# Kernel tuning notes

Measured on AMD Instinct MI355X. Metric: run time of the kernel, lower is better.

The kernel has to match this reference:

```python
import jax, jax.numpy as jnp
import numpy as np

N, E, G = 50000, 800000, 1024      # nodes, edges, graphs
NF, R, H, O, B = 32, 4, 64, 16, 2  # node vocab, relations, hidden, output, conv blocks
MAX_DEG = 10                       # PyG MFConv default max_degree


def setup_inputs() -> dict:
    key = jax.random.key(0)
    ks = jax.random.split(key, 32)
    s = 0.05
    inp = {
        "x": jax.random.normal(ks[0], (N, NF), jnp.float32),
        "edge_attr": jax.random.normal(ks[1], (E, R), jnp.float32),
        "edge_index": jax.random.randint(ks[2], (2, E), 0, N),
        "batch_idx": jnp.sort(jax.random.randint(ks[3], (N,), 0, G)),
        "emb": jax.random.normal(ks[4], (NF, H), jnp.float32) * s,
        "lin1_w": jax.random.normal(ks[5], (H, H), jnp.float32) * s,
        "lin1_b": jnp.zeros((H,), jnp.float32),
        "lin2_w": jax.random.normal(ks[6], (H, O), jnp.float32) * s,
        "lin2_b": jnp.zeros((O,), jnp.float32),
    }
    for b in range(B):
        k = 7 + 4 * b
        inp[f"rgcn_w{b}"] = jax.random.normal(ks[k], (R, H, H), jnp.float32) * s
        inp[f"rgcn_root{b}"] = jax.random.normal(ks[k + 1], (H, H), jnp.float32) * s
        inp[f"rgcn_b{b}"] = jnp.zeros((H,), jnp.float32)
        inp[f"mf_wl{b}"] = jax.random.normal(ks[k + 2], (MAX_DEG + 1, H, H), jnp.float32) * s
        inp[f"mf_bl{b}"] = jnp.zeros((MAX_DEG + 1, H), jnp.float32)
        inp[f"mf_wr{b}"] = jax.random.normal(ks[k + 3], (MAX_DEG + 1, H, H), jnp.float32) * s
    return inp


def _rgcn(h, src, tgt, rel, W, Wroot, bias):
    # PyG RGCNConv: per-relation linear transform + per-(node,relation) MEAN aggregation + root + bias.
    hx = jnp.einsum('nh,rho->rno', h, W)            # [R,N,H] transformed features per relation
    m = hx[rel, src]                                # [E,H] per-edge messages
    seg = tgt * R + rel                             # segment id per (target node, relation)
    cnt = jax.ops.segment_sum(jnp.ones((E,), h.dtype), seg, num_segments=N * R)
    inv = jnp.where(cnt > 0, 1.0 / cnt, 0.0)
    agg = jax.ops.segment_sum(m * inv[seg][:, None], tgt, num_segments=N)
    return agg + h @ Wroot + bias


def _mfconv(h, src, tgt, Wl, bl, Wr):
    # PyG MFConv: sum-aggregate neighbors, then degree-indexed linear layers (lin_l has bias, lin_r none).
    deg = jnp.clip(jax.ops.segment_sum(jnp.ones((E,), jnp.int32), tgt, num_segments=N), 0, MAX_DEG)
    agg = jax.ops.segment_sum(h[src], tgt, num_segments=N)   # [N,H]
    out = jnp.zeros_like(h)
    for d in range(MAX_DEG + 1):                    # fixed small set of degree buckets
        mask = (deg == d)[:, None]
        out = out + jnp.where(mask, agg @ Wl[d] + bl[d] + h @ Wr[d], 0.0)
    return out


def reference(x, edge_index, edge_attr, batch_idx, emb,
              rgcn_w0, rgcn_root0, rgcn_b0, mf_wl0, mf_bl0, mf_wr0,
              rgcn_w1, rgcn_root1, rgcn_b1, mf_wl1, mf_bl1, mf_wr1,
              lin1_w, lin1_b, lin2_w, lin2_b):
    src, tgt = edge_index[0], edge_index[1]
    rel = jnp.argmax(edge_attr, axis=-1)
    h = emb[jnp.argmax(x, axis=-1)]                 # node embedding lookup
    blocks = [(rgcn_w0, rgcn_root0, rgcn_b0, mf_wl0, mf_bl0, mf_wr0),
              (rgcn_w1, rgcn_root1, rgcn_b1, mf_wl1, mf_bl1, mf_wr1)]
    for (W, Wro, bi, Wl, bl, Wr) in blocks:
        h = jax.nn.relu(h)
        h = _rgcn(h, src, tgt, rel, W, Wro, bi)
        h = jax.nn.relu(h)
        h = _mfconv(h, src, tgt, Wl, bl, Wr)
    g = jax.ops.segment_sum(h, batch_idx, num_segments=G)   # global add pool
    g = jax.nn.relu(g @ lin1_w + lin1_b)
    return g @ lin2_w + lin2_b
```

## Files before the change

kernel.cpp:

```cpp
#include <hip/hip_runtime.h>
#include <hip/hip_fp16.h>
#include <cstdint>
#include <cstddef>

#define Nn 50000
#define Ne 800000
#define Ng 1024
#define NFd 32
#define Rr 4
#define Hd 64
#define Od 16
#define MAXD 10
#define NSEG (Nn * Rr)
#define SCAN_BLK ((NSEG + 255) / 256)
#define ORDER_SZ (Nn + 176)
#define NB_MF (ORDER_SZ / 16)
#define NB_RG (Nn / 16)
#define NB_RELSEG (Ne / 256)
#define NB_EMBED (Nn / 4)
#define WT_PER_LAYER (Hd * 5 * Hd)
#define MFWT_PER_LAYER ((MAXD + 1) * Hd * 2 * Hd)
#define PREP_TOTAL (2 * WT_PER_LAYER + 2 * MFWT_PER_LAYER)

typedef _Float16 f16x8 __attribute__((ext_vector_type(8)));
typedef float f32x4 __attribute__((ext_vector_type(4)));

__device__ __forceinline__ float reluf(float v) { return v > 0.f ? v : 0.f; }
__device__ __forceinline__ int rfl(int v) { return __builtin_amdgcn_readfirstlane(v); }

__global__ void k_rel_emb(const float4* __restrict__ ea, const int* __restrict__ eidx,
                          int* __restrict__ seg, int* __restrict__ rank,
                          int* __restrict__ cnt,
                          const float* __restrict__ x, const float* __restrict__ emb,
                          __half* __restrict__ h16) {
    if (blockIdx.x < NB_RELSEG) {
        int e = blockIdx.x * 256 + threadIdx.x;
        float4 a = ea[e];
        int bi = 0; float bv = a.x;
        if (a.y > bv) { bv = a.y; bi = 1; }
        if (a.z > bv) { bv = a.z; bi = 2; }
        if (a.w > bv) { bv = a.w; bi = 3; }
        int s = eidx[Ne + e] * Rr + bi;
        seg[e] = s;
        rank[e] = atomicAdd(&cnt[s], 1);
    } else {
        int wave = ((blockIdx.x - NB_RELSEG) * 256 + threadIdx.x) >> 6;
        int lane = threadIdx.x & 63;
        float v = (lane < NFd) ? x[(size_t)wave * NFd + lane] : -1e30f;
        int idx = lane;
        #pragma unroll
        for (int off = 16; off >= 1; off >>= 1) {
            float ov = __shfl_down(v, off);
            int oi = __shfl_down(idx, off);
            if (ov > v || (ov == v && oi < idx)) { v = ov; idx = oi; }
        }
        idx = __shfl(idx, 0);
        float hv = reluf(emb[(size_t)idx * Hd + lane]);
        h16[(size_t)wave * Hd + lane] = __float2half(hv);
    }
}

__global__ void k_prep(const float* __restrict__ w0, const float* __restrict__ r0,
                       const float* __restrict__ w1, const float* __restrict__ r1,
                       const float* __restrict__ wl0, const float* __restrict__ wr0,
                       const float* __restrict__ wl1, const float* __restrict__ wr1,
                       __half* __restrict__ wt, __half* __restrict__ mfwt) {
    int idx = blockIdx.x * 256 + threadIdx.x;
    if (idx < 2 * WT_PER_LAYER) {
        int b = idx / WT_PER_LAYER;
        int rem = idx % WT_PER_LAYER;
        int c = rem / 320;
        int k = rem % 320;
        const float* W  = b ? w1 : w0;
        const float* Rt = b ? r1 : r0;
        float v = (k < 64) ? Rt[k * Hd + c]
                           : W[((size_t)((k - 64) >> 6)) * Hd * Hd + ((k - 64) & 63) * Hd + c];
        wt[idx] = __float2half(v);
    } else if (idx < PREP_TOTAL) {
        int j = idx - 2 * WT_PER_LAYER;
        int b = j / MFWT_PER_LAYER;
        int rem = j % MFWT_PER_LAYER;
        int d = rem / (Hd * 128);
        int r2 = rem % (Hd * 128);
        int c = r2 / 128;
        int k = r2 % 128;
        const float* Wl = b ? wl1 : wl0;
        const float* Wr = b ? wr1 : wr0;
        float v = (k < 64) ? Wl[(size_t)d * Hd * Hd + k * Hd + c]
                           : Wr[(size_t)d * Hd * Hd + (k - 64) * Hd + c];
        mfwt[j] = __float2half(v);
    }
}

__global__ void k_scan1(const int* __restrict__ cnt, int* __restrict__ off,
                        int* __restrict__ bsum, int* __restrict__ bcnt) {
    __shared__ int s[256];
    __shared__ int hist[16];
    int t = threadIdx.x;
    if (t < 16) hist[t] = 0;
    int idx = blockIdx.x * 256 + t;
    int v = (idx < NSEG) ? cnt[idx] : 0;
    s[t] = v;
    __syncthreads();
    if ((t & 3) == 0 && idx < NSEG) {
        int dsum = s[t] + s[t + 1] + s[t + 2] + s[t + 3];
        atomicAdd(&hist[min(dsum, MAXD)], 1);
    }
    #pragma unroll
    for (int o = 1; o < 256; o <<= 1) {
        int x = (t >= o) ? s[t - o] : 0;
        __syncthreads();
        s[t] += x;
        __syncthreads();
    }
    if (idx < NSEG) off[idx] = s[t] - v;
    if (t == 255) bsum[blockIdx.x] = s[255];
    if (t < 16) {
        int h = hist[t];
        if (h > 0) atomicAdd(&bcnt[t], h);
    }
}

__global__ void k_scan2(int* __restrict__ bsum, const int* __restrict__ bcnt,
                        int* __restrict__ bbase, int* __restrict__ order) {
    __shared__ int s[1024];
    int t = threadIdx.x;
    int v = (t < SCAN_BLK) ? bsum[t] : 0;
    s[t] = v;
    __syncthreads();
    #pragma unroll
    for (int o = 1; o < 1024; o <<= 1) {
        int x = (t >= o) ? s[t - o] : 0;
        __syncthreads();
        s[t] += x;
        __syncthreads();
    }
    if (t < SCAN_BLK) bsum[t] = s[t] - v;
    if (t == 0) {
        int run = 0;
        for (int d = 0; d <= MAXD; d++) {
            int c = bcnt[d];
            bbase[d] = run;
            int pad = (c + 15) & ~15;
            for (int i = c; i < pad; i++) order[run + i] = -1;
            run += pad;
        }
        for (int i = run; i < ORDER_SZ; i++) order[i] = -1;
    }
}

__global__ void k_scan3_bucket(int* __restrict__ off, const int* __restrict__ bsum,
                               const int4* __restrict__ cnt4, const int* __restrict__ bbase,
                               int* __restrict__ bfill, int* __restrict__ order) {
    __shared__ int hist[16];
    __shared__ int base[16];
    int t = threadIdx.x;
    if (t < 16) hist[t] = 0;
    __syncthreads();
    int idx = blockIdx.x * 256 + t;
    if (idx == 0) off[NSEG] = Ne;
    if (idx < NSEG) off[idx] = off[idx] + bsum[blockIdx.x];
    int d = 0, rk = 0;
    bool valid = (idx < Nn);
    if (valid) {
        int4 c = cnt4[idx];
        d = min(c.x + c.y + c.z + c.w, MAXD);
        rk = atomicAdd(&hist[d], 1);
    }
    __syncthreads();
    if (t < 16) {
        int h = hist[t];
        base[t] = (h > 0) ? atomicAdd(&bfill[t], h) : 0;
    }
    __syncthreads();
    if (valid) order[bbase[d] + base[d] + rk] = idx | (d << 20);
}

__global__ void k_scatter(const int* __restrict__ eidx, const int* __restrict__ seg,
                          const int* __restrict__ rank, const int* __restrict__ off,
                          int* __restrict__ sorted_src) {
    int e = blockIdx.x * 256 + threadIdx.x;
    if (e >= Ne) return;
    int pos = off[seg[e]] + rank[e];
    sorted_src[pos] = eidx[e];
}

#define H16(ptr, s) __half2float((ptr)[(size_t)(s) * Hd + lane])

__global__ __launch_bounds__(256) void k_rgcn_fused(
        const __half* __restrict__ hin16,
        const int* __restrict__ off, const int* __restrict__ ssrc,
        const __half* __restrict__ wt, const float* __restrict__ bias,
        float* __restrict__ hout, __half* __restrict__ hout16) {
    __shared__ __align__(16) __half alds[16 * 296];
    int tid = threadIdx.x;
    int wv = tid >> 6, lane = tid & 63;
    int nblk = rfl(blockIdx.x * 16);
    int n0 = nblk + wv * 4;
    int obv = off[4 * n0 + min(lane, 16)];
    int cntv = __shfl(obv, lane + 1) - obv;
    float ivv = (cntv > 0) ? 1.f / (float)cntv : 0.f;
    int e    = rfl(__shfl(obv, 0));
    int eEnd = rfl(__shfl(obv, 16));

    float acc = 0.f, snap = 0.f;
    int segi = 0;
    int nb = rfl(__shfl(obv, 1));

#define EMIT_SEG do {                                                \
        float d_ = acc - snap; snap = acc;                           \
        float iv_ = __shfl(ivv, segi);                               \
        alds[(wv * 4 + (segi >> 2)) * 296 + (segi & 3) * 72 + lane]  \
            = __float2half(d_ * iv_);                                \
        segi++;                                                      \
        nb = (segi < 16) ? rfl(__shfl(obv, segi + 1)) : 0x7fffffff;  \
    } while (0)

    if (e + 16 <= eEnd) {
        int4 iA = *(const int4*)(ssrc + e);
        int4 iB = *(const int4*)(ssrc + e + 4);
        int4 iC = *(const int4*)(ssrc + e + 8);
        int4 iD = *(const int4*)(ssrc + e + 12);
        while (true) {
            int en = e + 16;
            bool more = (en + 16 <= eEnd);
            int4 jA, jB, jC, jD;
            if (more) {
                jA = *(const int4*)(ssrc + en);
                jB = *(const int4*)(ssrc + en + 4);
                jC = *(const int4*)(ssrc + en + 8);
                jD = *(const int4*)(ssrc + en + 12);
            }
            float v0 = H16(hin16, iA.x);
            float v1 = H16(hin16, iA.y);
            float v2 = H16(hin16, iA.z);
            float v3 = H16(hin16, iA.w);
            float v4 = H16(hin16, iB.x);
            float v5 = H16(hin16, iB.y);
            float v6 = H16(hin16, iB.z);
            float v7 = H16(hin16, iB.w);
            float v8 = H16(hin16, iC.x);
            float v9 = H16(hin16, iC.y);
            float vA = H16(hin16, iC.z);
            float vB = H16(hin16, iC.w);
            float vC = H16(hin16, iD.x);
            float vD = H16(hin16, iD.y);
            float vE = H16(hin16, iD.z);
            float vF = H16(hin16, iD.w);
            while (e + 0  == nb) EMIT_SEG;  acc += v0;
            while (e + 1  == nb) EMIT_SEG;  acc += v1;
            while (e + 2  == nb) EMIT_SEG;  acc += v2;
            while (e + 3  == nb) EMIT_SEG;  acc += v3;
            while (e + 4  == nb) EMIT_SEG;  acc += v4;
            while (e + 5  == nb) EMIT_SEG;  acc += v5;
            while (e + 6  == nb) EMIT_SEG;  acc += v6;
            while (e + 7  == nb) EMIT_SEG;  acc += v7;
            while (e + 8  == nb) EMIT_SEG;  acc += v8;
            while (e + 9  == nb) EMIT_SEG;  acc += v9;
            while (e + 10 == nb) EMIT_SEG;  acc += vA;
            while (e + 11 == nb) EMIT_SEG;  acc += vB;
            while (e + 12 == nb) EMIT_SEG;  acc += vC;
            while (e + 13 == nb) EMIT_SEG;  acc += vD;
            while (e + 14 == nb) EMIT_SEG;  acc += vE;
            while (e + 15 == nb) EMIT_SEG;  acc += vF;
            e = en;
            if (!more) break;
            iA = jA; iB = jB; iC = jC; iD = jD;
        }
    }
    for (; e < eEnd; e++) {
        while (e == nb) EMIT_SEG;
        int s = rfl(ssrc[e]);
        acc += H16(hin16, s);
    }
    while (segi < 16) EMIT_SEG;
#undef EMIT_SEG

    __syncthreads();

    int rp = lane & 15;
    int g  = lane >> 4;
    const __half* ha = hin16 + (size_t)(nblk + rp) * Hd + 8 * g;
    const __half* ba = wt + (size_t)(wv * 16 + rp) * 320 + 8 * g;
    const __half* aa = alds + rp * 296 + 8 * g;
    f32x4 dacc = {0.f, 0.f, 0.f, 0.f};
    #pragma unroll
    for (int s = 0; s < 10; s++) {
        f16x8 bfrag = *(const f16x8*)(ba + s * 32);
        f16x8 afrag;
        if (s < 2) afrag = *(const f16x8*)(ha + s * 32);
        else       afrag = *(const f16x8*)(aa + ((s - 2) >> 1) * 72 + ((s - 2) & 1) * 32);
        dacc = __builtin_amdgcn_mfma_f32_16x16x32_f16(afrag, bfrag, dacc, 0, 0, 0);
    }
    int c = wv * 16 + rp;
    float bb = bias[c];
    #pragma unroll
    for (int j = 0; j < 4; j++) {
        int row = nblk + g * 4 + j;
        float v = reluf(dacc[j] + bb);
        hout[(size_t)row * Hd + c] = v;
        hout16[(size_t)row * Hd + c] = __float2half(v);
    }
}

__global__ __launch_bounds__(256) void k_mf_fused(
        const __half* __restrict__ hin16,
        const int* __restrict__ off, const int* __restrict__ ssrc,
        const int* __restrict__ order, const __half* __restrict__ mfwt,
        const float* __restrict__ bl,
        float* __restrict__ hout, __half* __restrict__ hout16, int relu_out) {
    __shared__ __align__(16) __half alds[16 * 72];
    int tid = threadIdx.x;
    int wv = tid >> 6, lane = tid & 63;
    int blk = rfl(blockIdx.x * 16);
    int ent0 = rfl(order[blk]);
    if (ent0 < 0) return;
    int d = ent0 >> 20;
    for (int i = 0; i < 4; i++) {
        int slot = blk + wv * 4 + i;
        int ent = rfl(order[slot]);
        float sum = 0.f;
        if (ent >= 0) {
            int n = ent & 0xFFFFF;
            int e0 = rfl(off[n * Rr]);
            int e4 = rfl(off[n * Rr + Rr]);
            float p0 = 0.f, p1 = 0.f, p2 = 0.f, p3 = 0.f;
            int e = e0;
            for (; e + 16 <= e4; e += 16) {
                const int4 sA = *(const int4*)(ssrc + e);
                const int4 sB = *(const int4*)(ssrc + e + 4);
                const int4 sC = *(const int4*)(ssrc + e + 8);
                const int4 sD = *(const int4*)(ssrc + e + 12);
                p0 += H16(hin16, sA.x) + H16(hin16, sA.y) + H16(hin16, sA.z) + H16(hin16, sA.w);
                p1 += H16(hin16, sB.x) + H16(hin16, sB.y) + H16(hin16, sB.z) + H16(hin16, sB.w);
                p2 += H16(hin16, sC.x) + H16(hin16, sC.y) + H16(hin16, sC.z) + H16(hin16, sC.w);
                p3 += H16(hin16, sD.x) + H16(hin16, sD.y) + H16(hin16, sD.z) + H16(hin16, sD.w);
            }
            for (; e + 4 <= e4; e += 4) {
                const int4 sA = *(const int4*)(ssrc + e);
                p0 += H16(hin16, sA.x) + H16(hin16, sA.y) + H16(hin16, sA.z) + H16(hin16, sA.w);
            }
            for (; e < e4; e++) {
                int s = rfl(ssrc[e]);
                p0 += H16(hin16, s);
            }
            sum = (p0 + p1) + (p2 + p3);
        }
        alds[(wv * 4 + i) * 72 + lane] = __float2half(sum);
    }
    __syncthreads();

    int rp = lane & 15;
    int g  = lane >> 4;
    int entr = order[blk + rp];
    int nr = (entr >= 0) ? (entr & 0xFFFFF) : 0;
    const __half* aa = alds + rp * 72 + 8 * g;
    const __half* ha = hin16 + (size_t)nr * Hd + 8 * g;
    const __half* ba = mfwt + ((size_t)d * Hd + wv * 16 + rp) * 128 + 8 * g;
    f32x4 dacc = {0.f, 0.f, 0.f, 0.f};
    #pragma unroll
    for (int s = 0; s < 4; s++) {
        f16x8 bfrag = *(const f16x8*)(ba + s * 32);
        f16x8 afrag = (s < 2) ? *(const f16x8*)(aa + s * 32)
                              : *(const f16x8*)(ha + (s - 2) * 32);
        dacc = __builtin_amdgcn_mfma_f32_16x16x32_f16(afrag, bfrag, dacc, 0, 0, 0);
    }
    int c = wv * 16 + rp;
    float bb = bl[d * Hd + c];
    #pragma unroll
    for (int j = 0; j < 4; j++) {
        int entw = order[blk + g * 4 + j];
        if (entw >= 0) {
            int n = entw & 0xFFFFF;
            float v = dacc[j] + bb;
            if (relu_out) {
                v = reluf(v);
                hout16[(size_t)n * Hd + c] = __float2half(v);
            }
            hout[(size_t)n * Hd + c] = v;
        }
    }
}

__global__ void k_pool(const float* __restrict__ h, const int* __restrict__ batch,
                       float* __restrict__ g) {
    int wave = rfl((blockIdx.x * 256 + threadIdx.x) >> 6);
    int lane = threadIdx.x & 63;
    int n0 = wave * 4;
    if (n0 >= Nn) return;
    int b0 = batch[n0], b1 = batch[n0 + 1], b2 = batch[n0 + 2], b3 = batch[n0 + 3];
    float v0 = h[(size_t)n0 * Hd + lane];
    float v1 = h[(size_t)(n0 + 1) * Hd + lane];
    float v2 = h[(size_t)(n0 + 2) * Hd + lane];
    float v3 = h[(size_t)(n0 + 3) * Hd + lane];
    if (b0 == b1 && b0 == b2 && b0 == b3) {
        unsafeAtomicAdd(&g[(size_t)b0 * Hd + lane], v0 + v1 + v2 + v3);
    } else {
        unsafeAtomicAdd(&g[(size_t)b0 * Hd + lane], v0);
        unsafeAtomicAdd(&g[(size_t)b1 * Hd + lane], v1);
        unsafeAtomicAdd(&g[(size_t)b2 * Hd + lane], v2);
        unsafeAtomicAdd(&g[(size_t)b3 * Hd + lane], v3);
    }
}

__global__ void k_head(const float* __restrict__ g, const float* __restrict__ w1,
                       const float* __restrict__ b1, const float* __restrict__ w2,
                       const float* __restrict__ b2, float* __restrict__ out) {
    __shared__ float t[4][Hd];
    int wv = threadIdx.x >> 6;
    int lane = threadIdx.x & 63;
    int gi = blockIdx.x * 4 + wv;
    float acc = b1[lane];
    for (int k = 0; k < Hd; k++) acc += g[(size_t)gi * Hd + k] * w1[k * Hd + lane];
    t[wv][lane] = reluf(acc);
    __syncthreads();
    if (lane < Od) {
        float o = b2[lane];
        for (int k = 0; k < Hd; k++) o += t[wv][k] * w2[k * Od + lane];
        out[(size_t)gi * Od + lane] = o;
    }
}

extern "C" void kernel_launch(void* const* d_in, const int* in_sizes, int n_in,
                              void* d_out, int out_size, void* d_ws, size_t ws_size,
                              hipStream_t stream) {
    const float* x      = (const float*)d_in[0];
    const float* ea     = (const float*)d_in[1];
    const int*   eidx   = (const int*)d_in[2];
    const int*   batch  = (const int*)d_in[3];
    const float* emb    = (const float*)d_in[4];
    const float* lin1_w = (const float*)d_in[5];
    const float* lin1_b = (const float*)d_in[6];
    const float* lin2_w = (const float*)d_in[7];
    const float* lin2_b = (const float*)d_in[8];
    const float* rgcn_w[2]    = {(const float*)d_in[9],  (const float*)d_in[15]};
    const float* rgcn_root[2] = {(const float*)d_in[10], (const float*)d_in[16]};
    const float* rgcn_b[2]    = {(const float*)d_in[11], (const float*)d_in[17]};
    const float* mf_wl[2]     = {(const float*)d_in[12], (const float*)d_in[18]};
    const float* mf_bl[2]     = {(const float*)d_in[13], (const float*)d_in[19]};
    const float* mf_wr[2]     = {(const float*)d_in[14], (const float*)d_in[20]};

    char* p = (char*)d_ws;
    float* h0    = (float*)p; p += sizeof(float) * (size_t)Nn * Hd;
    float* h1    = (float*)p; p += sizeof(float) * (size_t)Nn * Hd;
    __half* h16a = (__half*)p; p += sizeof(__half) * (size_t)Nn * Hd;
    __half* h16b = (__half*)p; p += sizeof(__half) * (size_t)Nn * Hd;
    float* gbuf  = (float*)p; p += sizeof(float) * (size_t)Ng * Hd;
    __half* wt16 = (__half*)p; p += sizeof(__half) * (size_t)2 * WT_PER_LAYER;
    __half* mfwt16 = (__half*)p; p += sizeof(__half) * (size_t)2 * MFWT_PER_LAYER;
    int* seg     = (int*)p;   p += sizeof(int) * (size_t)Ne;
    int* rank    = (int*)p;   p += sizeof(int) * (size_t)Ne;
    int* ssrc    = (int*)p;   p += sizeof(int) * (size_t)Ne;
    int* cnt     = (int*)p;   p += sizeof(int) * (size_t)NSEG;
    int* bcnt    = (int*)p;   p += sizeof(int) * 16;
    int* bfill   = (int*)p;   p += sizeof(int) * 16;
    int* off     = (int*)p;   p += sizeof(int) * (size_t)(NSEG + 1);
    int* bsum    = (int*)p;   p += sizeof(int) * 1024;
    int* bbase   = (int*)p;   p += sizeof(int) * 16;
    int* order   = (int*)p;   p += sizeof(int) * (size_t)ORDER_SZ;

    hipMemsetAsync(cnt, 0, sizeof(int) * ((size_t)NSEG + 32), stream);
    hipMemsetAsync(gbuf, 0, sizeof(float) * (size_t)Ng * Hd, stream);

    k_prep<<<(PREP_TOTAL + 255) / 256, 256, 0, stream>>>(
        rgcn_w[0], rgcn_root[0], rgcn_w[1], rgcn_root[1],
        mf_wl[0], mf_wr[0], mf_wl[1], mf_wr[1], wt16, mfwt16);
    k_rel_emb<<<NB_RELSEG + NB_EMBED, 256, 0, stream>>>((const float4*)ea, eidx, seg, rank,
                                                        cnt, x, emb, h16a);
    k_scan1<<<SCAN_BLK, 256, 0, stream>>>(cnt, off, bsum, bcnt);
    k_scan2<<<1, 1024, 0, stream>>>(bsum, bcnt, bbase, order);
    k_scan3_bucket<<<SCAN_BLK, 256, 0, stream>>>(off, bsum, (const int4*)cnt, bbase,
                                                 bfill, order);
    k_scatter<<<Ne / 256, 256, 0, stream>>>(eidx, seg, rank, off, ssrc);

    float* h32a = h0;  float* h32b = h1;
    __half* hin16 = h16a;  __half* hout16 = h16b;
    for (int b = 0; b < 2; b++) {
        k_rgcn_fused<<<NB_RG, 256, 0, stream>>>(hin16, off, ssrc, wt16 + b * WT_PER_LAYER,
                                                rgcn_b[b], h32b, hout16);
        k_mf_fused<<<NB_MF, 256, 0, stream>>>(hout16, off, ssrc, order,
                                              mfwt16 + b * MFWT_PER_LAYER, mf_bl[b],
                                              h32a, hin16, b == 0 ? 1 : 0);
    }
    k_pool<<<Nn / 16, 256, 0, stream>>>(h32a, batch, gbuf);
    k_head<<<Ng / 4, 256, 0, stream>>>(gbuf, lin1_w, lin1_b, lin2_w, lin2_b, (float*)d_out);
}
```

Before: 345.7 us.

## Gather multiple edges per wave via packed half2 loads and drop redundant fp32 writes

The RGCN and MFConv gather loops now have each wave fetch several neighbor rows at once with packed half2/uint2 loads: half-waves take alternate edges, or quarter-waves take every fourth edge, and partial sums are merged with xor shuffles. The embedding kernel handles two nodes per wave with half2 stores. Edge scattering now uses an atomic fill cursor instead of a per-edge rank array, which removes the rank write and read. Unused fp32 hidden-state outputs are no longer written. In exchange there are more shuffles and more complex segment-boundary handling, and the scatter order within each segment becomes nondeterministic, which can change the floating-point summation order.

```diff
diff --git a/kernel.cpp b/kernel.cpp
--- a/kernel.cpp
+++ b/kernel.cpp
@@ -17,7 +17,7 @@
 #define NB_MF (ORDER_SZ / 16)
 #define NB_RG (Nn / 16)
 #define NB_RELSEG (Ne / 256)
-#define NB_EMBED (Nn / 4)
+#define NB_EMBED (Nn / 8)
 #define WT_PER_LAYER (Hd * 5 * Hd)
 #define MFWT_PER_LAYER ((MAXD + 1) * Hd * 2 * Hd)
 #define PREP_TOTAL (2 * WT_PER_LAYER + 2 * MFWT_PER_LAYER)
@@ -29,8 +29,7 @@
 __device__ __forceinline__ int rfl(int v) { return __builtin_amdgcn_readfirstlane(v); }
 
 __global__ void k_rel_emb(const float4* __restrict__ ea, const int* __restrict__ eidx,
-                          int* __restrict__ seg, int* __restrict__ rank,
-                          int* __restrict__ cnt,
+                          int* __restrict__ seg, int* __restrict__ cnt,
                           const float* __restrict__ x, const float* __restrict__ emb,
                           __half* __restrict__ h16) {
     if (blockIdx.x < NB_RELSEG) {
@@ -42,21 +41,24 @@
         if (a.w > bv) { bv = a.w; bi = 3; }
         int s = eidx[Ne + e] * Rr + bi;
         seg[e] = s;
-        rank[e] = atomicAdd(&cnt[s], 1);
+        atomicAdd(&cnt[s], 1);
     } else {
         int wave = ((blockIdx.x - NB_RELSEG) * 256 + threadIdx.x) >> 6;
         int lane = threadIdx.x & 63;
-        float v = (lane < NFd) ? x[(size_t)wave * NFd + lane] : -1e30f;
-        int idx = lane;
+        int h = lane >> 5, q = lane & 31;
+        int node = wave * 2 + h;
+        float v = x[(size_t)node * NFd + q];
+        int idx = q;
         #pragma unroll
-        for (int off = 16; off >= 1; off >>= 1) {
-            float ov = __shfl_down(v, off);
-            int oi = __shfl_down(idx, off);
+        for (int o = 16; o >= 1; o >>= 1) {
+            float ov = __shfl_xor(v, o);
+            int oi = __shfl_xor(idx, o);
             if (ov > v || (ov == v && oi < idx)) { v = ov; idx = oi; }
         }
-        idx = __shfl(idx, 0);
-        float hv = reluf(emb[(size_t)idx * Hd + lane]);
-        h16[(size_t)wave * Hd + lane] = __float2half(hv);
+        const float2* e2 = (const float2*)(emb + (size_t)idx * Hd);
+        float2 ev = e2[q];
+        ((__half2*)h16)[(size_t)node * 32 + q] =
+            __floats2half2_rn(reluf(ev.x), reluf(ev.y));
     }
 }
 
@@ -151,7 +153,8 @@
 
 __global__ void k_scan3_bucket(int* __restrict__ off, const int* __restrict__ bsum,
                                const int4* __restrict__ cnt4, const int* __restrict__ bbase,
-                               int* __restrict__ bfill, int* __restrict__ order) {
+                               int* __restrict__ bfill, int* __restrict__ order,
+                               int* __restrict__ fill) {
     __shared__ int hist[16];
     __shared__ int base[16];
     int t = threadIdx.x;
@@ -159,7 +162,11 @@
     __syncthreads();
     int idx = blockIdx.x * 256 + t;
     if (idx == 0) off[NSEG] = Ne;
-    if (idx < NSEG) off[idx] = off[idx] + bsum[blockIdx.x];
+    if (idx < NSEG) {
+        int v = off[idx] + bsum[blockIdx.x];
+        off[idx] = v;
+        fill[idx] = v;
+    }
     int d = 0, rk = 0;
     bool valid = (idx < Nn);
     if (valid) {
@@ -177,24 +184,22 @@
 }
 
 __global__ void k_scatter(const int* __restrict__ eidx, const int* __restrict__ seg,
-                          const int* __restrict__ rank, const int* __restrict__ off,
-                          int* __restrict__ sorted_src) {
+                          int* __restrict__ fill, int* __restrict__ sorted_src) {
     int e = blockIdx.x * 256 + threadIdx.x;
     if (e >= Ne) return;
-    int pos = off[seg[e]] + rank[e];
+    int pos = atomicAdd(&fill[seg[e]], 1);
     sorted_src[pos] = eidx[e];
 }
-
-#define H16(ptr, s) __half2float((ptr)[(size_t)(s) * Hd + lane])
 
 __global__ __launch_bounds__(256) void k_rgcn_fused(
         const __half* __restrict__ hin16,
         const int* __restrict__ off, const int* __restrict__ ssrc,
         const __half* __restrict__ wt, const float* __restrict__ bias,
-        float* __restrict__ hout, __half* __restrict__ hout16) {
+        __half* __restrict__ hout16) {
     __shared__ __align__(16) __half alds[16 * 296];
     int tid = threadIdx.x;
     int wv = tid >> 6, lane = tid & 63;
+    int h = lane >> 5, q = lane & 31;
     int nblk = rfl(blockIdx.x * 16);
     int n0 = nblk + wv * 4;
     int obv = off[4 * n0 + min(lane, 16)];
@@ -202,19 +207,35 @@
     float ivv = (cntv > 0) ? 1.f / (float)cntv : 0.f;
     int e    = rfl(__shfl(obv, 0));
     int eEnd = rfl(__shfl(obv, 16));
-
-    float acc = 0.f, snap = 0.f;
+    const __half2* hp = (const __half2*)hin16;
+
+    float ax = 0.f, ay = 0.f;
+    float px = 0.f, py = 0.f;
+    float vx = 0.f, vy = 0.f;
     int segi = 0;
     int nb = rfl(__shfl(obv, 1));
 
-#define EMIT_SEG do {                                                \
-        float d_ = acc - snap; snap = acc;                           \
+#define EMIT(SUB) do {                                               \
+        float dx = ax - px, dy = ay - py;                            \
+        float ox = ((SUB) && h) ? vx : 0.f;                          \
+        float oy = ((SUB) && h) ? vy : 0.f;                          \
+        dx -= ox; dy -= oy;                                          \
+        dx += __shfl_xor(dx, 32); dy += __shfl_xor(dy, 32);          \
         float iv_ = __shfl(ivv, segi);                               \
-        alds[(wv * 4 + (segi >> 2)) * 296 + (segi & 3) * 72 + lane]  \
-            = __float2half(d_ * iv_);                                \
+        if (lane < 32)                                               \
+            *(__half2*)&alds[(wv * 4 + (segi >> 2)) * 296            \
+                             + (segi & 3) * 72 + 2 * q]              \
+                = __floats2half2_rn(dx * iv_, dy * iv_);             \
+        px = ax - ox; py = ay - oy;                                  \
         segi++;                                                      \
         nb = (segi < 16) ? rfl(__shfl(obv, segi + 1)) : 0x7fffffff;  \
     } while (0)
+
+#define PSTEP(dj, t0) {                                              \
+        while ((t0) == nb) EMIT(0);                                  \
+        float2 f_ = __half22float2(dj);                              \
+        vx = f_.x; vy = f_.y; ax += f_.x; ay += f_.y;                \
+        while ((t0) + 1 == nb) EMIT(1); }
 
     if (e + 16 <= eEnd) {
         int4 iA = *(const int4*)(ssrc + e);
@@ -222,6 +243,22 @@
         int4 iC = *(const int4*)(ssrc + e + 8);
         int4 iD = *(const int4*)(ssrc + e + 12);
         while (true) {
+            int s0 = h ? iA.y : iA.x;
+            int s1 = h ? iA.w : iA.z;
+            int s2 = h ? iB.y : iB.x;
+            int s3 = h ? iB.w : iB.z;
+            int s4 = h ? iC.y : iC.x;
+            int s5 = h ? iC.w : iC.z;
+            int s6 = h ? iD.y : iD.x;
+            int s7 = h ? iD.w : iD.z;
+            __half2 d0 = hp[s0 * 32 + q];
+            __half2 d1 = hp[s1 * 32 + q];
+            __half2 d2 = hp[s2 * 32 + q];
+            __half2 d3 = hp[s3 * 32 + q];
+            __half2 d4 = hp[s4 * 32 + q];
+            __half2 d5 = hp[s5 * 32 + q];
+            __half2 d6 = hp[s6 * 32 + q];
+            __half2 d7 = hp[s7 * 32 + q];
             int en = e + 16;
             bool more = (en + 16 <= eEnd);
             int4 jA, jB, jC, jD;
@@ -231,50 +268,32 @@
                 jC = *(const int4*)(ssrc + en + 8);
                 jD = *(const int4*)(ssrc + en + 12);
             }
-            float v0 = H16(hin16, iA.x);
-            float v1 = H16(hin16, iA.y);
-            float v2 = H16(hin16, iA.z);
-            float v3 = H16(hin16, iA.w);
-            float v4 = H16(hin16, iB.x);
-            float v5 = H16(hin16, iB.y);
-            float v6 = H16(hin16, iB.z);
-            float v7 = H16(hin16, iB.w);
-            float v8 = H16(hin16, iC.x);
-            float v9 = H16(hin16, iC.y);
-            float vA = H16(hin16, iC.z);
-            float vB = H16(hin16, iC.w);
-            float vC = H16(hin16, iD.x);
-            float vD = H16(hin16, iD.y);
-            float vE = H16(hin16, iD.z);
-            float vF = H16(hin16, iD.w);
-            while (e + 0  == nb) EMIT_SEG;  acc += v0;
-            while (e + 1  == nb) EMIT_SEG;  acc += v1;
-            while (e + 2  == nb) EMIT_SEG;  acc += v2;
-            while (e + 3  == nb) EMIT_SEG;  acc += v3;
-            while (e + 4  == nb) EMIT_SEG;  acc += v4;
-            while (e + 5  == nb) EMIT_SEG;  acc += v5;
-            while (e + 6  == nb) EMIT_SEG;  acc += v6;
-            while (e + 7  == nb) EMIT_SEG;  acc += v7;
-            while (e + 8  == nb) EMIT_SEG;  acc += v8;
-            while (e + 9  == nb) EMIT_SEG;  acc += v9;
-            while (e + 10 == nb) EMIT_SEG;  acc += vA;
-            while (e + 11 == nb) EMIT_SEG;  acc += vB;
-            while (e + 12 == nb) EMIT_SEG;  acc += vC;
-            while (e + 13 == nb) EMIT_SEG;  acc += vD;
-            while (e + 14 == nb) EMIT_SEG;  acc += vE;
-            while (e + 15 == nb) EMIT_SEG;  acc += vF;
+            PSTEP(d0, e + 0)  PSTEP(d1, e + 2)  PSTEP(d2, e + 4)  PSTEP(d3, e + 6)
+            PSTEP(d4, e + 8)  PSTEP(d5, e + 10) PSTEP(d6, e + 12) PSTEP(d7, e + 14)
             e = en;
             if (!more) break;
             iA = jA; iB = jB; iC = jC; iD = jD;
         }
     }
-    for (; e < eEnd; e++) {
-        while (e == nb) EMIT_SEG;
-        int s = rfl(ssrc[e]);
-        acc += H16(hin16, s);
-    }
-    while (segi < 16) EMIT_SEG;
-#undef EMIT_SEG
+    for (; e + 2 <= eEnd; e += 2) {
+        while (e == nb) EMIT(0);
+        int sa = rfl(ssrc[e]), sb = rfl(ssrc[e + 1]);
+        int s = h ? sb : sa;
+        float2 f = __half22float2(hp[s * 32 + q]);
+        vx = f.x; vy = f.y; ax += f.x; ay += f.y;
+        while (e + 1 == nb) EMIT(1);
+    }
+    if (e < eEnd) {
+        while (e == nb) EMIT(0);
+        int sa = rfl(ssrc[e]);
+        float2 f = __half22float2(hp[sa * 32 + q]);
+        if (h) { f.x = 0.f; f.y = 0.f; }
+        ax += f.x; ay += f.y;
+        e++;
+    }
+    while (segi < 16) EMIT(0);
+#undef PSTEP
+#undef EMIT
 
     __syncthreads();
 
@@ -298,7 +317,6 @@
     for (int j = 0; j < 4; j++) {
         int row = nblk + g * 4 + j;
         float v = reluf(dacc[j] + bb);
-        hout[(size_t)row * Hd + c] = v;
         hout16[(size_t)row * Hd + c] = __float2half(v);
     }
 }
@@ -312,42 +330,68 @@
     __shared__ __align__(16) __half alds[16 * 72];
     int tid = threadIdx.x;
     int wv = tid >> 6, lane = tid & 63;
+    int g2 = lane >> 4, q4 = lane & 15;
     int blk = rfl(blockIdx.x * 16);
     int ent0 = rfl(order[blk]);
     if (ent0 < 0) return;
     int d = ent0 >> 20;
+    const uint2* hp2 = (const uint2*)hin16;
+
+#define SEL4(v4) ((g2 & 2) ? ((g2 & 1) ? (v4).w : (v4).z) : ((g2 & 1) ? (v4).y : (v4).x))
+#define ACC8(dw) { float2 f_ = __half22float2(*(__half2*)&(dw).x);   \
+                   float2 g_ = __half22float2(*(__half2*)&(dw).y);   \
+                   a0 += f_.x; a1 += f_.y; a2 += g_.x; a3 += g_.y; }
+
     for (int i = 0; i < 4; i++) {
         int slot = blk + wv * 4 + i;
         int ent = rfl(order[slot]);
-        float sum = 0.f;
+        float a0 = 0.f, a1 = 0.f, a2 = 0.f, a3 = 0.f;
         if (ent >= 0) {
             int n = ent & 0xFFFFF;
             int e0 = rfl(off[n * Rr]);
             int e4 = rfl(off[n * Rr + Rr]);
-            float p0 = 0.f, p1 = 0.f, p2 = 0.f, p3 = 0.f;
             int e = e0;
             for (; e + 16 <= e4; e += 16) {
-                const int4 sA = *(const int4*)(ssrc + e);
-                const int4 sB = *(const int4*)(ssrc + e + 4);
-                const int4 sC = *(const int4*)(ssrc + e + 8);
-                const int4 sD = *(const int4*)(ssrc + e + 12);
-                p0 += H16(hin16, sA.x) + H16(hin16, sA.y) + H16(hin16, sA.z) + H16(hin16, sA.w);
-                p1 += H16(hin16, sB.x) + H16(hin16, sB.y) + H16(hin16, sB.z) + H16(hin16, sB.w);
-                p2 += H16(hin16, sC.x) + H16(hin16, sC.y) + H16(hin16, sC.z) + H16(hin16, sC.w);
-                p3 += H16(hin16, sD.x) + H16(hin16, sD.y) + H16(hin16, sD.z) + H16(hin16, sD.w);
+                int4 iA = *(const int4*)(ssrc + e);
+                int4 iB = *(const int4*)(ssrc + e + 4);
+                int4 iC = *(const int4*)(ssrc + e + 8);
+                int4 iD = *(const int4*)(ssrc + e + 12);
+                int sA = SEL4(iA), sB = SEL4(iB), sC = SEL4(iC), sD = SEL4(iD);
+                uint2 dA = hp2[(size_t)sA * 16 + q4];
+                uint2 dB = hp2[(size_t)sB * 16 + q4];
+                uint2 dC = hp2[(size_t)sC * 16 + q4];
+                uint2 dD = hp2[(size_t)sD * 16 + q4];
+                ACC8(dA) ACC8(dB) ACC8(dC) ACC8(dD)
             }
             for (; e + 4 <= e4; e += 4) {
-                const int4 sA = *(const int4*)(ssrc + e);
-                p0 += H16(hin16, sA.x) + H16(hin16, sA.y) + H16(hin16, sA.z) + H16(hin16, sA.w);
+                int4 iA = *(const int4*)(ssrc + e);
+                int sA = SEL4(iA);
+                uint2 dA = hp2[(size_t)sA * 16 + q4];
+                ACC8(dA)
             }
-            for (; e < e4; e++) {
-                int s = rfl(ssrc[e]);
-                p0 += H16(hin16, s);
+            int rem = e4 - e;
+            if (rem > 0) {
+                int idxe = e + g2;
+                int sl = ssrc[(idxe < e4) ? idxe : (e4 - 1)];
+                uint2 dA = hp2[(size_t)sl * 16 + q4];
+                float2 f = __half22float2(*(__half2*)&dA.x);
+                float2 g = __half22float2(*(__half2*)&dA.y);
+                if (idxe >= e4) { f.x = 0.f; f.y = 0.f; g.x = 0.f; g.y = 0.f; }
+                a0 += f.x; a1 += f.y; a2 += g.x; a3 += g.y;
             }
-            sum = (p0 + p1) + (p2 + p3);
         }
-        alds[(wv * 4 + i) * 72 + lane] = __float2half(sum);
-    }
+        a0 += __shfl_xor(a0, 16); a0 += __shfl_xor(a0, 32);
+        a1 += __shfl_xor(a1, 16); a1 += __shfl_xor(a1, 32);
+        a2 += __shfl_xor(a2, 16); a2 += __shfl_xor(a2, 32);
+        a3 += __shfl_xor(a3, 16); a3 += __shfl_xor(a3, 32);
+        if (lane < 16) {
+            __half2* dst = (__half2*)&alds[(wv * 4 + i) * 72 + 4 * q4];
+            dst[0] = __floats2half2_rn(a0, a1);
+            dst[1] = __floats2half2_rn(a2, a3);
+        }
+    }
+#undef SEL4
+#undef ACC8
     __syncthreads();
 
     int rp = lane & 15;
@@ -373,11 +417,8 @@
         if (entw >= 0) {
             int n = entw & 0xFFFFF;
             float v = dacc[j] + bb;
-            if (relu_out) {
-                v = reluf(v);
-                hout16[(size_t)n * Hd + c] = __float2half(v);
-            }
-            hout[(size_t)n * Hd + c] = v;
+            if (relu_out) hout16[(size_t)n * Hd + c] = __float2half(reluf(v));
+            else          hout[(size_t)n * Hd + c] = v;
         }
     }
 }
@@ -441,16 +482,15 @@
     const float* mf_wr[2]     = {(const float*)d_in[14], (const float*)d_in[20]};
 
     char* p = (char*)d_ws;
-    float* h0    = (float*)p; p += sizeof(float) * (size_t)Nn * Hd;
-    float* h1    = (float*)p; p += sizeof(float) * (size_t)Nn * Hd;
+    float* h32   = (float*)p; p += sizeof(float) * (size_t)Nn * Hd;
     __half* h16a = (__half*)p; p += sizeof(__half) * (size_t)Nn * Hd;
     __half* h16b = (__half*)p; p += sizeof(__half) * (size_t)Nn * Hd;
     float* gbuf  = (float*)p; p += sizeof(float) * (size_t)Ng * Hd;
     __half* wt16 = (__half*)p; p += sizeof(__half) * (size_t)2 * WT_PER_LAYER;
     __half* mfwt16 = (__half*)p; p += sizeof(__half) * (size_t)2 * MFWT_PER_LAYER;
     int* seg     = (int*)p;   p += sizeof(int) * (size_t)Ne;
-    int* rank    = (int*)p;   p += sizeof(int) * (size_t)Ne;
     int* ssrc    = (int*)p;   p += sizeof(int) * (size_t)Ne;
+    int* fill    = (int*)p;   p += sizeof(int) * (size_t)NSEG;
     int* cnt     = (int*)p;   p += sizeof(int) * (size_t)NSEG;
     int* bcnt    = (int*)p;   p += sizeof(int) * 16;
     int* bfill   = (int*)p;   p += sizeof(int) * 16;
@@ -465,23 +505,22 @@
     k_prep<<<(PREP_TOTAL + 255) / 256, 256, 0, stream>>>(
         rgcn_w[0], rgcn_root[0], rgcn_w[1], rgcn_root[1],
         mf_wl[0], mf_wr[0], mf_wl[1], mf_wr[1], wt16, mfwt16);
-    k_rel_emb<<<NB_RELSEG + NB_EMBED, 256, 0, stream>>>((const float4*)ea, eidx, seg, rank,
+    k_rel_emb<<<NB_RELSEG + NB_EMBED, 256, 0, stream>>>((const float4*)ea, eidx, seg,
                                                         cnt, x, emb, h16a);
     k_scan1<<<SCAN_BLK, 256, 0, stream>>>(cnt, off, bsum, bcnt);
     k_scan2<<<1, 1024, 0, stream>>>(bsum, bcnt, bbase, order);
     k_scan3_bucket<<<SCAN_BLK, 256, 0, stream>>>(off, bsum, (const int4*)cnt, bbase,
-                                                 bfill, order);
-    k_scatter<<<Ne / 256, 256, 0, stream>>>(eidx, seg, rank, off, ssrc);
-
-    float* h32a = h0;  float* h32b = h1;
+                                                 bfill, order, fill);
+    k_scatter<<<Ne / 256, 256, 0, stream>>>(eidx, seg, fill, ssrc);
+
     __half* hin16 = h16a;  __half* hout16 = h16b;
     for (int b = 0; b < 2; b++) {
         k_rgcn_fused<<<NB_RG, 256, 0, stream>>>(hin16, off, ssrc, wt16 + b * WT_PER_LAYER,
-                                                rgcn_b[b], h32b, hout16);
+                                                rgcn_b[b], hout16);
         k_mf_fused<<<NB_MF, 256, 0, stream>>>(hout16, off, ssrc, order,
                                               mfwt16 + b * MFWT_PER_LAYER, mf_bl[b],
-                                              h32a, hin16, b == 0 ? 1 : 0);
-    }
-    k_pool<<<Nn / 16, 256, 0, stream>>>(h32a, batch, gbuf);
+                                              h32, hin16, b == 0 ? 1 : 0);
+    }
+    k_pool<<<Nn / 16, 256, 0, stream>>>(h32, batch, gbuf);
     k_head<<<Ng / 4, 256, 0, stream>>>(gbuf, lin1_w, lin1_b, lin2_w, lin2_b, (float*)d_out);
 }
```

After: 365.2 us. +5.6%, slower.
